# Performance work log

Measured on AMD Instinct MI355X. Metric: run time of the kernel, lower is better.

## Reference

```python
import jax, jax.numpy as jnp
import numpy as np

EPS = 1e-5

def _layernorm(x, gamma, beta):
    mu = jnp.mean(x, axis=-1, keepdims=True)
    var = jnp.var(x, axis=-1, keepdims=True)
    return (x - mu) * jax.lax.rsqrt(var + EPS) * gamma + beta

def setup_inputs() -> dict:
    key = jax.random.key(0)
    ks = jax.random.split(key, 8)
    B, I, H = 8192, 1024, 1024
    s_w = 1.0 / np.sqrt(I)
    s_u = 1.0 / np.sqrt(H)
    return {
        "x": jax.random.normal(ks[0], (B, I), jnp.float32),
        "h": jax.random.normal(ks[1], (B, H), jnp.float32),
        "c": jax.random.normal(ks[2], (B, H), jnp.float32),
        "W_w": jax.random.uniform(ks[3], (I, 4 * H), jnp.float32, -s_w, s_w),
        "W_b": jax.random.uniform(ks[4], (4 * H,), jnp.float32, -s_w, s_w),
        "U_w": jax.random.uniform(ks[5], (H, 4 * H), jnp.float32, -s_u, s_u),
        "ln_g_gamma": jnp.ones((4 * H,), jnp.float32),
        "ln_g_beta": jnp.zeros((4 * H,), jnp.float32),
        "ln_c_gamma": jnp.ones((H,), jnp.float32),
        "ln_c_beta": jnp.zeros((H,), jnp.float32),
    }

def reference(x, h, c, W_w, W_b, U_w, ln_g_gamma, ln_g_beta, ln_c_gamma, ln_c_beta):
    gates_x = x @ W_w + W_b            # [B, 4H]
    gates_h = h @ U_w                  # [B, 4H]
    gates = gates_x + gates_h + gates_x * gates_h  # multiplicative integration
    gates = _layernorm(gates, ln_g_gamma, ln_g_beta)
    i, f, g, o = jnp.split(gates, 4, axis=-1)
    i = jax.nn.sigmoid(i)
    f = jax.nn.sigmoid(f)
    o = jax.nn.sigmoid(o)
    g = jnp.tanh(g)
    c_new = f * c + i * g
    c_new = _layernorm(c_new, ln_c_gamma, ln_c_beta)
    h_new = o * jnp.tanh(c_new)
    return (h_new, h_new, c_new)
```

## Files before the change

kernel.cpp:

```cpp
#include <hip/hip_runtime.h>
#include <hip/hip_fp16.h>
#include <cstdint>


#define MB (1024ull * 1024ull)

typedef short bf16x8 __attribute__((ext_vector_type(8)));
typedef float f32x4  __attribute__((ext_vector_type(4)));

__device__ __forceinline__ bool bf16_mode(const void* g1) {
    return ((const unsigned short*)g1)[0] == 0x3F80u;
}
__device__ __forceinline__ float b2f(unsigned short u) {
    union { unsigned int i; float f; } v; v.i = ((unsigned int)u) << 16; return v.f;
}
__device__ __forceinline__ unsigned short f2b(float f) {
    unsigned int i = __float_as_uint(f);
    unsigned int r = (i + 0x7FFFu + ((i >> 16) & 1u)) >> 16;
    return (unsigned short)r;
}
__device__ __forceinline__ unsigned short f2h(float f) {
    __half h = __float2half_rn(f);
    return *(unsigned short*)&h;
}
__device__ __forceinline__ void uph8(uint4 v, float* o) {
    unsigned int w[4] = { v.x, v.y, v.z, v.w };
#pragma unroll
    for (int q = 0; q < 4; ++q) {
        __half2 h = *(__half2*)&w[q];
        float2 f = __half22float2(h);
        o[2 * q] = f.x; o[2 * q + 1] = f.y;
    }
}
__device__ __forceinline__ void up4(uint2 v, float* o) {
    o[0] = __uint_as_float(v.x << 16);
    o[1] = __uint_as_float(v.x & 0xFFFF0000u);
    o[2] = __uint_as_float(v.y << 16);
    o[3] = __uint_as_float(v.y & 0xFFFF0000u);
}
__device__ __forceinline__ unsigned int pack2(unsigned short a, unsigned short b) {
    return (unsigned int)a | ((unsigned int)b << 16);
}
__device__ __forceinline__ void ld4(const void* p, size_t idx, bool isbf, float* o) {
    if (isbf) up4(*(const uint2*)((const unsigned short*)p + idx), o);
    else { float4 v = *(const float4*)((const float*)p + idx); o[0]=v.x; o[1]=v.y; o[2]=v.z; o[3]=v.w; }
}
__device__ __forceinline__ float fast_sigmoid(float z) { return 1.f / (1.f + __expf(-z)); }
__device__ __forceinline__ float fast_tanh(float z)    { return 1.f - 2.f / (__expf(2.f * z) + 1.f); }

__device__ __forceinline__ void load_lds16(const unsigned short* g, unsigned short* l) {
    __builtin_amdgcn_global_load_lds(
        (const __attribute__((address_space(1))) unsigned int*)g,
        (__attribute__((address_space(3))) unsigned int*)l,
        16, 0, 0);
}

__global__ __launch_bounds__(256)
void prep_weights(const void* __restrict__ Ww, const void* __restrict__ Uw,
                  const void* __restrict__ g1,
                  unsigned short* __restrict__ Wt, unsigned short* __restrict__ Ut)
{
    const bool isbf = bf16_mode(g1);
    const void* src = blockIdx.z ? Uw : Ww;
    unsigned short* dst = blockIdx.z ? Ut : Wt;
    __shared__ unsigned short tile[64][68];
    const int t  = threadIdx.x;
    const int tx = t & 15;
    const int ty = t >> 4;
    const int bx = blockIdx.x * 64;
    const int by = blockIdx.y * 64;
    if (isbf) {
        const unsigned short* s = (const unsigned short*)src;
#pragma unroll
        for (int it = 0; it < 4; ++it) {
            const int r = ty + it * 16;
            uint2 v = *(const uint2*)(s + (size_t)(by + r) * 4096 + bx + tx * 4);
            tile[r][tx * 4 + 0] = (unsigned short)(v.x & 0xFFFFu);
            tile[r][tx * 4 + 1] = (unsigned short)(v.x >> 16);
            tile[r][tx * 4 + 2] = (unsigned short)(v.y & 0xFFFFu);
            tile[r][tx * 4 + 3] = (unsigned short)(v.y >> 16);
        }
    } else {
        const float* s = (const float*)src;
#pragma unroll
        for (int it = 0; it < 4; ++it) {
            const int r = ty + it * 16;
            float4 v = *(const float4*)(s + (size_t)(by + r) * 4096 + bx + tx * 4);
            tile[r][tx * 4 + 0] = f2b(v.x);
            tile[r][tx * 4 + 1] = f2b(v.y);
            tile[r][tx * 4 + 2] = f2b(v.z);
            tile[r][tx * 4 + 3] = f2b(v.w);
        }
    }
    __syncthreads();
#pragma unroll
    for (int it = 0; it < 4; ++it) {
        const int rn = ty + it * 16;
        const int ck = tx * 4;
        uint2 w;
        w.x = pack2(tile[ck + 0][rn], tile[ck + 1][rn]);
        w.y = pack2(tile[ck + 2][rn], tile[ck + 3][rn]);
        *(uint2*)(dst + (size_t)(bx + rn) * 1024 + by + ck) = w;
    }
}

__global__ __launch_bounds__(256)
void prep_xh(const void* __restrict__ X, const void* __restrict__ Hs,
             const void* __restrict__ g1, void* __restrict__ outb)
{
    if (bf16_mode(g1)) return;
    const float* src = (blockIdx.y == 0) ? (const float*)X : (const float*)Hs;
    unsigned short* dst = (unsigned short*)((char*)outb + (blockIdx.y == 0 ? 48 * MB : 80 * MB));
    const size_t i0 = ((size_t)blockIdx.x * 256 + threadIdx.x) * 8;
    float4 a = *(const float4*)(src + i0);
    float4 b = *(const float4*)(src + i0 + 4);
    uint4 o;
    o.x = pack2(f2b(a.x), f2b(a.y));
    o.y = pack2(f2b(a.z), f2b(a.w));
    o.z = pack2(f2b(b.x), f2b(b.y));
    o.w = pack2(f2b(b.z), f2b(b.w));
    *(uint4*)(dst + i0) = o;
}

__global__ __launch_bounds__(512, 2)
void milstm_gemm(const void* __restrict__ Xraw, const void* __restrict__ Hraw,
                 const void* __restrict__ g1, const void* __restrict__ outb,
                 const unsigned short* __restrict__ Wt,
                 const unsigned short* __restrict__ Ut,
                 unsigned short* __restrict__ Gx, unsigned short* __restrict__ Gh,
                 int m0)
{
    const bool isbf = bf16_mode(g1);
    const int  z    = blockIdx.z;
    const unsigned short* A = z
        ? (isbf ? (const unsigned short*)Hraw : (const unsigned short*)((const char*)outb + 80 * MB))
        : (isbf ? (const unsigned short*)Xraw : (const unsigned short*)((const char*)outb + 48 * MB));
    const unsigned short* Bm = z ? Ut : Wt;
    unsigned short* Gout = z ? Gh : Gx;

    __shared__ __align__(16) unsigned short ldsA[2][2][8192];
    __shared__ __align__(16) unsigned short ldsB[2][2][8192];

    const int t    = threadIdx.x;
    const int wave = t >> 6;
    const int lane = t & 63;
    const int quad = lane >> 4;
    const int l16  = lane & 15;
    const int wm   = wave >> 2;
    const int wn   = wave & 3;

    const int nwg  = gridDim.x * gridDim.y;
    const int wgid = blockIdx.y * gridDim.x + blockIdx.x;
    const int swz  = (wgid & 7) * (nwg >> 3) + (wgid >> 3);
    const int bm   = (swz >> 4) * 256;
    const int bn   = (swz & 15) * 256;

    const int gls = (((t & 7) ^ ((t >> 3) & 7)) * 8);
    const unsigned short* pA = A  + (size_t)(m0 + bm + (t >> 3)) * 1024 + gls;
    const unsigned short* pB = Bm + (size_t)(bn + (t >> 3)) * 1024 + gls;

#define ST_A(DB, H, KO) do {                                                  \
        load_lds16(pA + (H) * 131072 + (KO),         &ldsA[DB][H][t * 8]);    \
        load_lds16(pA + (H) * 131072 + 65536 + (KO), &ldsA[DB][H][4096 + t * 8]); \
    } while (0)
#define ST_B(DB, H, KO) do {                                                  \
        load_lds16(pB + (H) * 131072 + (KO),         &ldsB[DB][H][t * 8]);    \
        load_lds16(pB + (H) * 131072 + 65536 + (KO), &ldsB[DB][H][4096 + t * 8]); \
    } while (0)

    const int gp0 = ((quad)     ^ (l16 & 7)) * 8;
    const int gp1 = ((4 + quad) ^ (l16 & 7)) * 8;
    const unsigned short* bA0 = &ldsA[0][wm][0] + l16 * 64;
    const unsigned short* bA1 = &ldsA[1][wm][0] + l16 * 64;
    const unsigned short* bB0 = &ldsB[0][wn >> 1][0] + (wn & 1) * 4096 + l16 * 64;
    const unsigned short* bB1 = &ldsB[1][wn >> 1][0] + (wn & 1) * 4096 + l16 * 64;

#define LD_AF(BASE) do { _Pragma("unroll")                                    \
        for (int j = 0; j < 4; ++j) {                                         \
            aF[j * 2 + 0] = *(const bf16x8*)((BASE) + j * 1024 + gp0);        \
            aF[j * 2 + 1] = *(const bf16x8*)((BASE) + j * 1024 + gp1);        \
        } } while (0)
#define LD_BF(BASE, DST) do { _Pragma("unroll")                               \
        for (int n = 0; n < 2; ++n) {                                         \
            DST[n * 2 + 0] = *(const bf16x8*)((BASE) + n * 1024 + gp0);       \
            DST[n * 2 + 1] = *(const bf16x8*)((BASE) + n * 1024 + gp1);       \
        } } while (0)

#define BAR()   __builtin_amdgcn_s_barrier()
#define LGKM0() do { asm volatile("s_waitcnt lgkmcnt(0)" ::: "memory");       \
                     __builtin_amdgcn_sched_barrier(0); } while (0)
#define MFMA16(MBASE, NBASE, BV) do {                                         \
        __builtin_amdgcn_s_setprio(1);                                        \
        _Pragma("unroll")                                                     \
        for (int j = 0; j < 4; ++j)                                           \
            _Pragma("unroll")                                                 \
            for (int n = 0; n < 2; ++n)                                       \
                _Pragma("unroll")                                             \
                for (int ks = 0; ks < 2; ++ks)                                \
                    acc[(MBASE) + j][(NBASE) + n] =                           \
                        __builtin_amdgcn_mfma_f32_16x16x32_bf16(              \
                            aF[j * 2 + ks], BV[n * 2 + ks],                   \
                            acc[(MBASE) + j][(NBASE) + n], 0, 0, 0);          \
        __builtin_amdgcn_s_setprio(0);                                        \
    } while (0)

    f32x4 acc[8][4] = {};
    bf16x8 aF[8], bL[4], bH[4];

    ST_A(0, 0, 0);  ST_B(0, 0, 0);  ST_B(0, 1, 0);  ST_A(0, 1, 0);
    ST_A(1, 0, 64); ST_B(1, 0, 64); ST_B(1, 1, 64);
    asm volatile("s_waitcnt vmcnt(6)" ::: "memory");
    BAR();

    for (int i = 0; i < 8; ++i) {
        const int kt1 = (128 * i + 64)  & 1023;
        const int kt2 = (128 * i + 128) & 1023;
        const int kt3 = (128 * i + 192) & 1023;

        LD_AF(bA0); LD_BF(bB0, bL);
        ST_A(1, 1, kt1);
        BAR(); LGKM0();
        MFMA16(0, 0, bL);
        BAR();
        LD_BF(bB0 + 2048, bH);
        BAR(); LGKM0();
        MFMA16(0, 2, bH);
        BAR();
        LD_AF(bA0 + 4096);
        ST_B(0, 0, kt2);
        BAR(); LGKM0();
        MFMA16(4, 2, bH);
        BAR();
        ST_B(0, 1, kt2); ST_A(0, 0, kt2);
        BAR(); LGKM0();
        MFMA16(4, 0, bL);
        asm volatile("s_waitcnt vmcnt(6)" ::: "memory");
        BAR();
        LD_AF(bA1); LD_BF(bB1, bL);
        ST_A(0, 1, kt2);
        BAR(); LGKM0();
        MFMA16(0, 0, bL);
        BAR();
        LD_BF(bB1 + 2048, bH);
        BAR(); LGKM0();
        MFMA16(0, 2, bH);
        BAR();
        LD_AF(bA1 + 4096);
        ST_B(1, 0, kt3);
        BAR(); LGKM0();
        MFMA16(4, 2, bH);
        BAR();
        ST_B(1, 1, kt3); ST_A(1, 0, kt3);
        BAR(); LGKM0();
        MFMA16(4, 0, bL);
        asm volatile("s_waitcnt vmcnt(6)" ::: "memory");
        BAR();
    }
#undef ST_A
#undef ST_B
#undef LD_AF
#undef LD_BF
#undef BAR
#undef LGKM0
#undef MFMA16

    const int col0 = bn + wn * 64 + l16;
#pragma unroll
    for (int mi = 0; mi < 8; ++mi) {
        const int row0 = bm + wm * 128 + mi * 16 + quad * 4;
#pragma unroll
        for (int ni = 0; ni < 4; ++ni) {
            const int col = col0 + ni * 16;
#pragma unroll
            for (int r = 0; r < 4; ++r)
                Gout[(size_t)(row0 + r) * 4096 + col] = f2h(acc[mi][ni][r]);
        }
    }
}

__global__ __launch_bounds__(256)
void milstm_cell(const unsigned short* __restrict__ Gx,
                 const unsigned short* __restrict__ Gh,
                 const void* __restrict__ Wbr,
                 const void* __restrict__ C,
                 const void* __restrict__ g1, const void* __restrict__ b1,
                 const void* __restrict__ g2, const void* __restrict__ b2,
                 void* __restrict__ outb, int m0)
{
    const bool isbf = bf16_mode(g1);
    const int lrow = blockIdx.x;
    const int row  = m0 + lrow;
    const int tid  = threadIdx.x;
    const int lane = tid & 63;
    const int wave = tid >> 6;
    const uint4* gx4 = (const uint4*)(Gx + (size_t)lrow * 4096);
    const uint4* gh4 = (const uint4*)(Gh + (size_t)lrow * 4096);

    __shared__ __align__(16) float srow[4096];
    __shared__ float red[16];

    float s = 0.f, ss = 0.f;
#pragma unroll
    for (int u = 0; u < 2; ++u) {
        const int gbase = (tid * 2 + u) * 8;
        float fx[8], fh[8], bb[8];
        uph8(gx4[tid * 2 + u], fx);
        uph8(gh4[tid * 2 + u], fh);
        ld4(Wbr, gbase, isbf, bb);
        ld4(Wbr, gbase + 4, isbf, bb + 4);
        float g[8];
#pragma unroll
        for (int k = 0; k < 8; ++k) {
            const float ax = fx[k] + bb[k];
            const float v  = ax + fh[k] + ax * fh[k];
            g[k] = v;
            s  += v;
            ss += v * v;
        }
        *(float4*)&srow[gbase]     = make_float4(g[0], g[1], g[2], g[3]);
        *(float4*)&srow[gbase + 4] = make_float4(g[4], g[5], g[6], g[7]);
    }
#pragma unroll
    for (int off = 32; off > 0; off >>= 1) {
        s  += __shfl_xor(s, off, 64);
        ss += __shfl_xor(ss, off, 64);
    }
    if (lane == 0) { red[wave] = s; red[8 + wave] = ss; }
    __syncthreads();
    s  = red[0] + red[1] + red[2] + red[3];
    ss = red[8] + red[9] + red[10] + red[11];
    const float mu   = s * (1.f / 4096.f);
    const float rstd = rsqrtf(fmaxf(ss * (1.f / 4096.f) - mu * mu, 0.f) + 1e-5f);

    const int j0 = tid * 4;
    float xi[4], xf[4], xg[4], cc[4];
    float G1[4], B1[4], ii[4], cn[4], ov[4];

    { float4 v = *(const float4*)&srow[j0];        xi[0]=v.x; xi[1]=v.y; xi[2]=v.z; xi[3]=v.w; }
    { float4 v = *(const float4*)&srow[1024 + j0]; xf[0]=v.x; xf[1]=v.y; xf[2]=v.z; xf[3]=v.w; }
    { float4 v = *(const float4*)&srow[2048 + j0]; xg[0]=v.x; xg[1]=v.y; xg[2]=v.z; xg[3]=v.w; }
    { float4 v = *(const float4*)&srow[3072 + j0]; ov[0]=v.x; ov[1]=v.y; ov[2]=v.z; ov[3]=v.w; }
    ld4(C, (size_t)row * 1024 + j0, isbf, cc);

    ld4(g1, j0, isbf, G1); ld4(b1, j0, isbf, B1);
#pragma unroll
    for (int q = 0; q < 4; ++q) ii[q] = fast_sigmoid((xi[q] - mu) * rstd * G1[q] + B1[q]);
    ld4(g1, 1024 + j0, isbf, G1); ld4(b1, 1024 + j0, isbf, B1);
#pragma unroll
    for (int q = 0; q < 4; ++q) xf[q] = fast_sigmoid((xf[q] - mu) * rstd * G1[q] + B1[q]);
    ld4(g1, 2048 + j0, isbf, G1); ld4(b1, 2048 + j0, isbf, B1);
#pragma unroll
    for (int q = 0; q < 4; ++q) xg[q] = fast_tanh((xg[q] - mu) * rstd * G1[q] + B1[q]);
    ld4(g1, 3072 + j0, isbf, G1); ld4(b1, 3072 + j0, isbf, B1);
#pragma unroll
    for (int q = 0; q < 4; ++q) ov[q] = fast_sigmoid((ov[q] - mu) * rstd * G1[q] + B1[q]);
#pragma unroll
    for (int q = 0; q < 4; ++q) cn[q] = xf[q] * cc[q] + ii[q] * xg[q];

    float s2  = cn[0] + cn[1] + cn[2] + cn[3];
    float ss2 = cn[0]*cn[0] + cn[1]*cn[1] + cn[2]*cn[2] + cn[3]*cn[3];
#pragma unroll
    for (int off = 32; off > 0; off >>= 1) {
        s2  += __shfl_xor(s2, off, 64);
        ss2 += __shfl_xor(ss2, off, 64);
    }
    if (lane == 0) { red[4 + wave] = s2; red[12 + wave] = ss2; }
    __syncthreads();
    s2  = red[4]  + red[5]  + red[6]  + red[7];
    ss2 = red[12] + red[13] + red[14] + red[15];
    const float mu2   = s2 * (1.f / 1024.f);
    const float rstd2 = rsqrtf(fmaxf(ss2 * (1.f / 1024.f) - mu2 * mu2, 0.f) + 1e-5f);

    ld4(g2, j0, isbf, G1);
    ld4(b2, j0, isbf, B1);

    float hv[4], cv[4];
#pragma unroll
    for (int q = 0; q < 4; ++q) {
        cv[q] = (cn[q] - mu2) * rstd2 * G1[q] + B1[q];
        hv[q] = ov[q] * fast_tanh(cv[q]);
    }

    const size_t BH = (size_t)8192 * 1024;
    if (isbf) {
        unsigned short* out = (unsigned short*)outb;
        uint2 hb, cb;
        hb.x = pack2(f2b(hv[0]), f2b(hv[1])); hb.y = pack2(f2b(hv[2]), f2b(hv[3]));
        cb.x = pack2(f2b(cv[0]), f2b(cv[1])); cb.y = pack2(f2b(cv[2]), f2b(cv[3]));
        *(uint2*)(out + (size_t)row * 1024 + j0)          = hb;
        *(uint2*)(out + BH + (size_t)row * 1024 + j0)     = hb;
        *(uint2*)(out + 2 * BH + (size_t)row * 1024 + j0) = cb;
    } else {
        float* out = (float*)outb;
        float4 hf = { hv[0], hv[1], hv[2], hv[3] };
        float4 cf = { cv[0], cv[1], cv[2], cv[3] };
        *(float4*)(out + (size_t)row * 1024 + j0)          = hf;
        *(float4*)(out + BH + (size_t)row * 1024 + j0)     = hf;
        *(float4*)(out + 2 * BH + (size_t)row * 1024 + j0) = cf;
    }
}

extern "C" void kernel_launch(void* const* d_in, const int* in_sizes, int n_in,
                              void* d_out, int out_size, void* d_ws, size_t ws_size,
                              hipStream_t stream)
{
    const void* X  = d_in[0];
    const void* Hh = d_in[1];
    const void* C  = d_in[2];
    const void* Ww = d_in[3];
    const void* Wb = d_in[4];
    const void* Uw = d_in[5];
    const void* g1 = d_in[6];
    const void* b1 = d_in[7];
    const void* g2 = d_in[8];
    const void* b2 = d_in[9];

    const int P  = (ws_size >= 144 * MB) ? 1 : ((ws_size >= 80 * MB) ? 2 : 4);
    const int MR = 8192 / P;
    const size_t gsz = (size_t)MR * 4096;
    unsigned short* Gx = (unsigned short*)d_ws;
    unsigned short* Gh = Gx + gsz;
    unsigned short* Wt = Gh + gsz;
    unsigned short* Ut = Wt + (size_t)4096 * 1024;

    prep_weights<<<dim3(64, 16, 2), 256, 0, stream>>>(Ww, Uw, g1, Wt, Ut);
    prep_xh<<<dim3(4096, 2), 256, 0, stream>>>(X, Hh, g1, d_out);

    for (int ph = 0; ph < P; ++ph) {
        const int m0 = ph * MR;
        milstm_gemm<<<dim3(16, MR / 256, 2), 512, 0, stream>>>(
            X, Hh, g1, d_out, Wt, Ut, Gx, Gh, m0);
        milstm_cell<<<dim3(MR), 256, 0, stream>>>(
            Gx, Gh, Wb, C, g1, b1, g2, b2, d_out, m0);
    }
}
```

Baseline: 418.5 us.

## Double-buffer A fragments in registers to overlap LDS reads with MFMA

```diff
diff --git a/kernel.cpp b/kernel.cpp
--- a/kernel.cpp
+++ b/kernel.cpp
@@ -175,21 +175,22 @@
     const unsigned short* bB0 = &ldsB[0][wn >> 1][0] + (wn & 1) * 4096 + l16 * 64;
     const unsigned short* bB1 = &ldsB[1][wn >> 1][0] + (wn & 1) * 4096 + l16 * 64;
 
-#define LD_AF(BASE) do { _Pragma("unroll")                                    \
+#define LD_A8(DST, BASE) do { _Pragma("unroll")                               \
         for (int j = 0; j < 4; ++j) {                                         \
-            aF[j * 2 + 0] = *(const bf16x8*)((BASE) + j * 1024 + gp0);        \
-            aF[j * 2 + 1] = *(const bf16x8*)((BASE) + j * 1024 + gp1);        \
+            DST[j * 2 + 0] = *(const bf16x8*)((BASE) + j * 1024 + gp0);       \
+            DST[j * 2 + 1] = *(const bf16x8*)((BASE) + j * 1024 + gp1);       \
         } } while (0)
-#define LD_BF(BASE, DST) do { _Pragma("unroll")                               \
+#define LD_B4(DST, BASE) do { _Pragma("unroll")                               \
         for (int n = 0; n < 2; ++n) {                                         \
             DST[n * 2 + 0] = *(const bf16x8*)((BASE) + n * 1024 + gp0);       \
             DST[n * 2 + 1] = *(const bf16x8*)((BASE) + n * 1024 + gp1);       \
         } } while (0)
 
 #define BAR()   __builtin_amdgcn_s_barrier()
-#define LGKM0() do { asm volatile("s_waitcnt lgkmcnt(0)" ::: "memory");       \
-                     __builtin_amdgcn_sched_barrier(0); } while (0)
-#define MFMA16(MBASE, NBASE, BV) do {                                         \
+#define SB()    __builtin_amdgcn_sched_barrier(0)
+#define WAITLG(N) do { asm volatile("s_waitcnt lgkmcnt(" #N ")" ::: "memory"); SB(); } while (0)
+#define VM2()   asm volatile("s_waitcnt vmcnt(2)" ::: "memory")
+#define MFMA16(AV, MBASE, NBASE, BV) do {                                     \
         __builtin_amdgcn_s_setprio(1);                                        \
         _Pragma("unroll")                                                     \
         for (int j = 0; j < 4; ++j)                                           \
@@ -199,69 +200,77 @@
                 for (int ks = 0; ks < 2; ++ks)                                \
                     acc[(MBASE) + j][(NBASE) + n] =                           \
                         __builtin_amdgcn_mfma_f32_16x16x32_bf16(              \
-                            aF[j * 2 + ks], BV[n * 2 + ks],                   \
+                            AV[j * 2 + ks], BV[n * 2 + ks],                   \
                             acc[(MBASE) + j][(NBASE) + n], 0, 0, 0);          \
         __builtin_amdgcn_s_setprio(0);                                        \
     } while (0)
 
     f32x4 acc[8][4] = {};
-    bf16x8 aF[8], bL[4], bH[4];
-
-    ST_A(0, 0, 0);  ST_B(0, 0, 0);  ST_B(0, 1, 0);  ST_A(0, 1, 0);
-    ST_A(1, 0, 64); ST_B(1, 0, 64); ST_B(1, 1, 64);
+    bf16x8 aA[8], aB[8], bL[4], bH[4];
+
+    ST_A(0, 0, 0);  ST_A(0, 1, 0);  ST_B(0, 0, 0);  ST_B(0, 1, 0);
+    ST_B(1, 0, 64); ST_B(1, 1, 64); ST_A(1, 0, 64);
     asm volatile("s_waitcnt vmcnt(6)" ::: "memory");
     BAR();
+    LD_A8(aA, bA0);
+    LD_B4(bL, bB0);
 
     for (int i = 0; i < 8; ++i) {
         const int kt1 = (128 * i + 64)  & 1023;
         const int kt2 = (128 * i + 128) & 1023;
         const int kt3 = (128 * i + 192) & 1023;
 
-        LD_AF(bA0); LD_BF(bB0, bL);
+        LD_B4(bH, bB0 + 2048);
         ST_A(1, 1, kt1);
-        BAR(); LGKM0();
-        MFMA16(0, 0, bL);
-        BAR();
-        LD_BF(bB0 + 2048, bH);
-        BAR(); LGKM0();
-        MFMA16(0, 2, bH);
-        BAR();
-        LD_AF(bA0 + 4096);
+        BAR(); WAITLG(4);
+        MFMA16(aA, 0, 0, bL);
+        BAR();
+        LD_A8(aB, bA0 + 4096);
+        BAR(); WAITLG(8);
+        MFMA16(aA, 0, 2, bH);
+        BAR();
         ST_B(0, 0, kt2);
-        BAR(); LGKM0();
-        MFMA16(4, 2, bH);
+        BAR(); WAITLG(0);
+        MFMA16(aB, 4, 2, bH);
+        VM2();
         BAR();
         ST_B(0, 1, kt2); ST_A(0, 0, kt2);
-        BAR(); LGKM0();
-        MFMA16(4, 0, bL);
-        asm volatile("s_waitcnt vmcnt(6)" ::: "memory");
-        BAR();
-        LD_AF(bA1); LD_BF(bB1, bL);
+        LD_A8(aA, bA1);
+        SB();
+        BAR();
+        MFMA16(aB, 4, 0, bL);
+        LD_B4(bL, bB1);
+        BAR();
+        LD_B4(bH, bB1 + 2048);
         ST_A(0, 1, kt2);
-        BAR(); LGKM0();
-        MFMA16(0, 0, bL);
-        BAR();
-        LD_BF(bB1 + 2048, bH);
-        BAR(); LGKM0();
-        MFMA16(0, 2, bH);
-        BAR();
-        LD_AF(bA1 + 4096);
+        BAR(); WAITLG(4);
+        MFMA16(aA, 0, 0, bL);
+        BAR();
+        LD_A8(aB, bA1 + 4096);
+        BAR(); WAITLG(8);
+        MFMA16(aA, 0, 2, bH);
+        BAR();
         ST_B(1, 0, kt3);
-        BAR(); LGKM0();
-        MFMA16(4, 2, bH);
+        BAR(); WAITLG(0);
+        MFMA16(aB, 4, 2, bH);
+        VM2();
         BAR();
         ST_B(1, 1, kt3); ST_A(1, 0, kt3);
-        BAR(); LGKM0();
-        MFMA16(4, 0, bL);
-        asm volatile("s_waitcnt vmcnt(6)" ::: "memory");
+        LD_A8(aA, bA0);
+        SB();
+        BAR();
+        MFMA16(aB, 4, 0, bL);
+        LD_B4(bL, bB0);
         BAR();
     }
 #undef ST_A
 #undef ST_B
-#undef LD_AF
-#undef LD_BF
+#undef LD_A8
+#undef LD_B4
 #undef BAR
-#undef LGKM0
+#undef SB
+#undef WAITLG
+#undef VM2
 #undef MFMA16
 
     const int col0 = bn + wn * 64 + l16;
```

Measured after the change: 422.6 us. Within noise of the previous version (+1.0%).
